# Performance work log

Hardware: AMD Instinct MI355X
Metric: run time of the kernel (lower is better)

## Reference

```python
import jax, jax.numpy as jnp
import numpy as np

# Module config (matches init_kwargs)
IC, OC, K, R, C, STRIDE = 128, 256, 3, 64, 64, 1
TAPS = 576
B = 16
BIAS_LEN = 128
H_OUT = (R - K) // STRIDE + 1  # 62
W_OUT = (C - K) // STRIDE + 1  # 62


def setup_inputs() -> dict:
    key = jax.random.key(0)
    k1, k2, k3 = jax.random.split(key, 3)
    rng = np.random.default_rng(0)
    # Per output channel, choose TAPS distinct (c, ky, kx) taps out of IC*K*K.
    all_taps = IC * K * K
    tap_ids = np.stack([rng.choice(all_taps, TAPS, replace=False) for _ in range(OC)])  # [OC, TAPS]
    c = tap_ids // (K * K)
    rem = tap_ids % (K * K)
    ky, kx = rem // K, rem % K
    # Flattened gather index into a [IC, R, C] image, exactly as the CUDA module builds it.
    image_weight_index = (c * (R * C) + ky * C + kx).astype(np.int32).reshape(-1)  # [OC*TAPS]
    filter_lengths = np.full(OC, TAPS, dtype=np.int32)
    start_points = (np.arange(OC, dtype=np.int64) * TAPS).astype(np.int32)
    bias_index = rng.choice(OC, BIAS_LEN, replace=False).astype(np.int32)
    return {
        "images": jax.random.normal(k1, (B, IC, R, C), jnp.float32),
        "weight_value": jax.random.normal(k2, (OC * TAPS,), jnp.float32) * 0.05,
        "image_weight_index": jnp.asarray(image_weight_index),
        "filter_lengths": jnp.asarray(filter_lengths),
        "start_points": jnp.asarray(start_points),
        "bias_index": jnp.asarray(bias_index),
        "bias_value": jax.random.normal(k3, (BIAS_LEN,), jnp.float32),
    }


def reference(images, weight_value, image_weight_index, filter_lengths, start_points, bias_index, bias_value):
    nnz = weight_value.shape[0]
    # Taps are stored contiguously per output channel (start_points = cumsum of filter_lengths).
    oc_ids = jnp.repeat(jnp.arange(OC), filter_lengths, total_repeat_length=nnz)
    # Decode flattened image index back to (in_channel, ky, kx).
    c = image_weight_index // (R * C)
    rem = image_weight_index % (R * C)
    ky, kx = rem // C, rem % C
    # Scatter sparse taps into a dense OIHW kernel; the gather-conv math is then
    # an exact VALID strided cross-correlation.
    W = jnp.zeros((OC, IC, K, K), images.dtype).at[oc_ids, c, ky, kx].add(weight_value)
    out = jax.lax.conv_general_dilated(
        images, W, window_strides=(STRIDE, STRIDE), padding="VALID",
        dimension_numbers=("NCHW", "OIHW", "NCHW"))  # [B, OC, H_OUT, W_OUT]
    # Conditional bias: channel oc gets bias_value[j] for each j with bias_index[j] == oc.
    bias = jnp.zeros((OC,), images.dtype).at[bias_index].add(bias_value)
    return out + bias[None, :, None, None]
```

## Files before the change

kernel.cpp:

```cpp
#include <hip/hip_runtime.h>
#include <stdint.h>

#define IC 128
#define OC 256
#define RR 64
#define CCOLS 64
#define HO 62
#define WO 62
#define NB 16

#define W9T_BYTES (9 * OC * IC * 2)
#define CHUNK_STRIDE 8192
#define LDS_TOTAL (49152 + 1024)

typedef __bf16 bf16x8 __attribute__((ext_vector_type(8)));
typedef float f32x16 __attribute__((ext_vector_type(16)));

__device__ __forceinline__ unsigned short f2bf(float f) {
    unsigned u = __builtin_bit_cast(unsigned, f);
    u += 0x7FFFu + ((u >> 16) & 1u);
    return (unsigned short)(u >> 16);
}

__global__ void prep_weights(const float* __restrict__ wv,
                             const int* __restrict__ iwi,
                             const int* __restrict__ flen,
                             const int* __restrict__ sp,
                             unsigned char* __restrict__ W9Tf,
                             const int* __restrict__ bias_index,
                             const float* __restrict__ bias_value,
                             float* __restrict__ bias_dense, int nbias) {
    if (blockIdx.x == OC) {
        int t = threadIdx.x;
        if (t < OC) bias_dense[t] = 0.f;
        __syncthreads();
        if (t < nbias) atomicAdd(&bias_dense[bias_index[t]], bias_value[t]);
        return;
    }
    const int oc = blockIdx.x;
    const int s = sp[oc];
    const int n = flen[oc];
    const int g = oc >> 5;
    for (int t = threadIdx.x; t < n; t += blockDim.x) {
        const int ix = iwi[s + t];
        const int c = ix >> 12;
        const int rem = ix & 4095;
        const int ky = rem >> 6, kx = rem & 63;
        const int kp = ky * 3 + kx;
        const int ck = c >> 4;
        const int khalf = (c >> 3) & 1;
        const int lane = (oc & 31) + (khalf << 5);
        const size_t off = (size_t)(kp * 8 + ck) * CHUNK_STRIDE +
                           g * 1024 + lane * 16 + (c & 7) * 2;
        *(unsigned short*)(W9Tf + off) = f2bf(wv[s + t]);
    }
}

#define KSTEP1(IDX, AV, VN, LGN)                                              \
  {                                                                           \
    if constexpr ((IDX) + 1 < 72) {                                           \
      constexpr int i1_ = (IDX) + 1;                                          \
      constexpr int kp1_ = i1_ >> 3, ck1_ = i1_ & 7;                          \
      constexpr int o1_ = (kp1_ / 3) * 16384 + ck1_ * 2048 + (kp1_ % 3) * 16; \
      asm volatile("ds_read_b128 %0, %1" : "=v"(b0n) : "v"(bB + o1_));        \
      asm volatile("ds_read_b128 %0, %1" : "=v"(b1n) : "v"(bB + o1_ + 512));  \
    }                                                                         \
    asm volatile("s_waitcnt vmcnt(" VN ") lgkmcnt(" LGN ")" : "+v"(AV));      \
    __builtin_amdgcn_sched_barrier(0);                                        \
    acc0 = __builtin_amdgcn_mfma_f32_32x32x16_bf16(AV, b0c, acc0, 0, 0, 0);   \
    acc1 = __builtin_amdgcn_mfma_f32_32x32x16_bf16(AV, b1c, acc1, 0, 0, 0);   \
    if constexpr ((IDX) + 4 < 72)                                             \
      asm volatile("global_load_dwordx4 %0, %1, off"                          \
                   : "=v"(AV)                                                 \
                   : "v"(pA + (size_t)((IDX) + 4) * CHUNK_STRIDE));           \
    if constexpr ((IDX) + 1 < 72) { b0c = b0n; b1c = b1n; }                   \
  }

#define K4(I) KSTEP1((I)+0, aS0, "3", "2") KSTEP1((I)+1, aS1, "3", "2") \
              KSTEP1((I)+2, aS2, "3", "2") KSTEP1((I)+3, aS3, "3", "2")

__global__ __launch_bounds__(512, 2) void conv_mfma(
    const float* __restrict__ images,
    const unsigned char* __restrict__ W9Tf,
    const float* __restrict__ bias_dense,
    float* __restrict__ out)
{
    const int y = blockIdx.x;
    const int b = blockIdx.y;
    const int t = threadIdx.x;
    const int w = t >> 6;
    const int l = t & 63;
    const int lm = l & 31;
    const int lhi = l >> 5;

    __shared__ unsigned char lds[LDS_TOTAL];

    const float* __restrict__ imgb = images + (size_t)b * (IC * RR * CCOLS);

    {
        const int xs = t & 63;
        const int oct = t >> 6;
        #pragma unroll
        for (int krow = 0; krow < 3; ++krow) {
            #pragma unroll
            for (int h = 0; h < 2; ++h) {
                const int o = oct + 8 * h;
                const int c0 = o * 8;
                const float* __restrict__ p =
                    imgb + (size_t)c0 * (RR * CCOLS) + (y + krow) * CCOLS + xs;
                unsigned v0, v1, v2, v3;
                v0 = (unsigned)f2bf(p[0])              | ((unsigned)f2bf(p[RR * CCOLS])     << 16);
                v1 = (unsigned)f2bf(p[2 * RR * CCOLS]) | ((unsigned)f2bf(p[3 * RR * CCOLS]) << 16);
                v2 = (unsigned)f2bf(p[4 * RR * CCOLS]) | ((unsigned)f2bf(p[5 * RR * CCOLS]) << 16);
                v3 = (unsigned)f2bf(p[6 * RR * CCOLS]) | ((unsigned)f2bf(p[7 * RR * CCOLS]) << 16);
                *(uint4*)(lds + krow * 16384 + o * 1024 + xs * 16) =
                    make_uint4(v0, v1, v2, v3);
            }
        }
    }

    const unsigned char* __restrict__ pA = W9Tf + w * 1024 + l * 16;
    const unsigned bB = (unsigned)(uintptr_t)(lds + lhi * 1024 + lm * 16);

    __syncthreads();

    bf16x8 aS0, aS1, aS2, aS3, b0c, b1c, b0n, b1n;
    asm volatile("global_load_dwordx4 %0, %1, off" : "=v"(aS0) : "v"(pA));
    asm volatile("global_load_dwordx4 %0, %1, off" : "=v"(aS1) : "v"(pA + CHUNK_STRIDE));
    asm volatile("global_load_dwordx4 %0, %1, off" : "=v"(aS2) : "v"(pA + 2 * CHUNK_STRIDE));
    asm volatile("global_load_dwordx4 %0, %1, off" : "=v"(aS3) : "v"(pA + 3 * CHUNK_STRIDE));
    asm volatile("ds_read_b128 %0, %1" : "=v"(b0c) : "v"(bB));
    asm volatile("ds_read_b128 %0, %1" : "=v"(b1c) : "v"(bB + 512u));

    f32x16 acc0 = {}, acc1 = {};

    K4(0) K4(4) K4(8) K4(12) K4(16) K4(20) K4(24) K4(28) K4(32)
    K4(36) K4(40) K4(44) K4(48) K4(52) K4(56) K4(60) K4(64)
    KSTEP1(68, aS0, "3", "2") KSTEP1(69, aS1, "2", "2")
    KSTEP1(70, aS2, "1", "2") KSTEP1(71, aS3, "0", "0")

    const int ocw = 32 * w;
    #pragma unroll
    for (int r = 0; r < 16; ++r) {
        const int oc = ocw + (r & 3) + 8 * (r >> 2) + 4 * lhi;
        const float bv = bias_dense[oc];
        const size_t ob = (((size_t)b * OC + oc) * HO + y) * WO;
        out[ob + lm] = acc0[r] + bv;
        if (lm < 30)
            out[ob + 32 + lm] = acc1[r] + bv;
    }
}

extern "C" void kernel_launch(void* const* d_in, const int* in_sizes, int n_in,
                              void* d_out, int out_size, void* d_ws, size_t ws_size,
                              hipStream_t stream) {
    const float* images             = (const float*)d_in[0];
    const float* weight_value       = (const float*)d_in[1];
    const int*   image_weight_index = (const int*)d_in[2];
    const int*   filter_lengths     = (const int*)d_in[3];
    const int*   start_points       = (const int*)d_in[4];
    const int*   bias_index         = (const int*)d_in[5];
    const float* bias_value         = (const float*)d_in[6];
    float* out = (float*)d_out;

    unsigned char* W9Tf = (unsigned char*)d_ws;
    float* bias_dense = (float*)((char*)d_ws + W9T_BYTES);

    hipMemsetAsync(d_ws, 0, W9T_BYTES, stream);
    prep_weights<<<OC + 1, 256, 0, stream>>>(weight_value, image_weight_index,
                                             filter_lengths, start_points, W9Tf,
                                             bias_index, bias_value, bias_dense,
                                             in_sizes[5]);

    dim3 grid(HO, NB);
    conv_mfma<<<grid, 512, 0, stream>>>(images, W9Tf, bias_dense, out);
}
```

Baseline: 64.74 us.

## Halve block size and give each wave two output-channel tiles

Blocks shrink from 512 to 256 threads, and each of the four waves now computes two 32-channel M tiles. Each LDS-read B fragment is reused across two MFMAs, which halves LDS traffic per MFMA and doubles the weight loads kept in flight per wave. LDS use per block drops slightly and launch bounds move to 3 blocks per CU. The cost is more accumulator and A registers per wave, and fewer waves per block to share the image-tile staging.

```diff
diff --git a/kernel.cpp b/kernel.cpp
--- a/kernel.cpp
+++ b/kernel.cpp
@@ -11,7 +11,7 @@
 
 #define W9T_BYTES (9 * OC * IC * 2)
 #define CHUNK_STRIDE 8192
-#define LDS_TOTAL (49152 + 1024)
+#define LDS_TOTAL 49216
 
 typedef __bf16 bf16x8 __attribute__((ext_vector_type(8)));
 typedef float f32x16 __attribute__((ext_vector_type(16)));
@@ -56,7 +56,7 @@
     }
 }
 
-#define KSTEP1(IDX, AV, VN, LGN)                                              \
+#define KSTEP1(IDX, AV0, AV1, VN, LGN)                                        \
   {                                                                           \
     if constexpr ((IDX) + 1 < 72) {                                           \
       constexpr int i1_ = (IDX) + 1;                                          \
@@ -65,21 +65,30 @@
       asm volatile("ds_read_b128 %0, %1" : "=v"(b0n) : "v"(bB + o1_));        \
       asm volatile("ds_read_b128 %0, %1" : "=v"(b1n) : "v"(bB + o1_ + 512));  \
     }                                                                         \
-    asm volatile("s_waitcnt vmcnt(" VN ") lgkmcnt(" LGN ")" : "+v"(AV));      \
+    asm volatile("s_waitcnt vmcnt(" VN ") lgkmcnt(" LGN ")"                   \
+                 : "+v"(AV0), "+v"(AV1));                                     \
     __builtin_amdgcn_sched_barrier(0);                                        \
-    acc0 = __builtin_amdgcn_mfma_f32_32x32x16_bf16(AV, b0c, acc0, 0, 0, 0);   \
-    acc1 = __builtin_amdgcn_mfma_f32_32x32x16_bf16(AV, b1c, acc1, 0, 0, 0);   \
-    if constexpr ((IDX) + 4 < 72)                                             \
+    c00 = __builtin_amdgcn_mfma_f32_32x32x16_bf16(AV0, b0c, c00, 0, 0, 0);    \
+    c10 = __builtin_amdgcn_mfma_f32_32x32x16_bf16(AV1, b0c, c10, 0, 0, 0);    \
+    c01 = __builtin_amdgcn_mfma_f32_32x32x16_bf16(AV0, b1c, c01, 0, 0, 0);    \
+    c11 = __builtin_amdgcn_mfma_f32_32x32x16_bf16(AV1, b1c, c11, 0, 0, 0);    \
+    if constexpr ((IDX) + 4 < 72) {                                           \
       asm volatile("global_load_dwordx4 %0, %1, off"                          \
-                   : "=v"(AV)                                                 \
-                   : "v"(pA + (size_t)((IDX) + 4) * CHUNK_STRIDE));           \
+                   : "=v"(AV0)                                                \
+                   : "v"(pA0 + (size_t)((IDX) + 4) * CHUNK_STRIDE));          \
+      asm volatile("global_load_dwordx4 %0, %1, off"                          \
+                   : "=v"(AV1)                                                \
+                   : "v"(pA1 + (size_t)((IDX) + 4) * CHUNK_STRIDE));          \
+    }                                                                         \
     if constexpr ((IDX) + 1 < 72) { b0c = b0n; b1c = b1n; }                   \
   }
 
-#define K4(I) KSTEP1((I)+0, aS0, "3", "2") KSTEP1((I)+1, aS1, "3", "2") \
-              KSTEP1((I)+2, aS2, "3", "2") KSTEP1((I)+3, aS3, "3", "2")
+#define K4(I) KSTEP1((I)+0, a0S0, a1S0, "6", "2") \
+              KSTEP1((I)+1, a0S1, a1S1, "6", "2") \
+              KSTEP1((I)+2, a0S2, a1S2, "6", "2") \
+              KSTEP1((I)+3, a0S3, a1S3, "6", "2")
 
-__global__ __launch_bounds__(512, 2) void conv_mfma(
+__global__ __launch_bounds__(256, 3) void conv_mfma(
     const float* __restrict__ images,
     const unsigned char* __restrict__ W9Tf,
     const float* __restrict__ bias_dense,
@@ -99,12 +108,12 @@
 
     {
         const int xs = t & 63;
-        const int oct = t >> 6;
+        const int og = t >> 6;
         #pragma unroll
         for (int krow = 0; krow < 3; ++krow) {
             #pragma unroll
-            for (int h = 0; h < 2; ++h) {
-                const int o = oct + 8 * h;
+            for (int h = 0; h < 4; ++h) {
+                const int o = og + 4 * h;
                 const int c0 = o * 8;
                 const float* __restrict__ p =
                     imgb + (size_t)c0 * (RR * CCOLS) + (y + krow) * CCOLS + xs;
@@ -119,35 +128,46 @@
         }
     }
 
-    const unsigned char* __restrict__ pA = W9Tf + w * 1024 + l * 16;
+    const unsigned char* __restrict__ pA0 = W9Tf + (2 * w + 0) * 1024 + l * 16;
+    const unsigned char* __restrict__ pA1 = W9Tf + (2 * w + 1) * 1024 + l * 16;
     const unsigned bB = (unsigned)(uintptr_t)(lds + lhi * 1024 + lm * 16);
 
     __syncthreads();
 
-    bf16x8 aS0, aS1, aS2, aS3, b0c, b1c, b0n, b1n;
-    asm volatile("global_load_dwordx4 %0, %1, off" : "=v"(aS0) : "v"(pA));
-    asm volatile("global_load_dwordx4 %0, %1, off" : "=v"(aS1) : "v"(pA + CHUNK_STRIDE));
-    asm volatile("global_load_dwordx4 %0, %1, off" : "=v"(aS2) : "v"(pA + 2 * CHUNK_STRIDE));
-    asm volatile("global_load_dwordx4 %0, %1, off" : "=v"(aS3) : "v"(pA + 3 * CHUNK_STRIDE));
+    bf16x8 a0S0, a0S1, a0S2, a0S3, a1S0, a1S1, a1S2, a1S3;
+    bf16x8 b0c, b1c, b0n, b1n;
+    asm volatile("global_load_dwordx4 %0, %1, off" : "=v"(a0S0) : "v"(pA0));
+    asm volatile("global_load_dwordx4 %0, %1, off" : "=v"(a1S0) : "v"(pA1));
+    asm volatile("global_load_dwordx4 %0, %1, off" : "=v"(a0S1) : "v"(pA0 + CHUNK_STRIDE));
+    asm volatile("global_load_dwordx4 %0, %1, off" : "=v"(a1S1) : "v"(pA1 + CHUNK_STRIDE));
+    asm volatile("global_load_dwordx4 %0, %1, off" : "=v"(a0S2) : "v"(pA0 + 2 * CHUNK_STRIDE));
+    asm volatile("global_load_dwordx4 %0, %1, off" : "=v"(a1S2) : "v"(pA1 + 2 * CHUNK_STRIDE));
+    asm volatile("global_load_dwordx4 %0, %1, off" : "=v"(a0S3) : "v"(pA0 + 3 * CHUNK_STRIDE));
+    asm volatile("global_load_dwordx4 %0, %1, off" : "=v"(a1S3) : "v"(pA1 + 3 * CHUNK_STRIDE));
     asm volatile("ds_read_b128 %0, %1" : "=v"(b0c) : "v"(bB));
     asm volatile("ds_read_b128 %0, %1" : "=v"(b1c) : "v"(bB + 512u));
 
-    f32x16 acc0 = {}, acc1 = {};
+    f32x16 c00 = {}, c01 = {}, c10 = {}, c11 = {};
 
     K4(0) K4(4) K4(8) K4(12) K4(16) K4(20) K4(24) K4(28) K4(32)
     K4(36) K4(40) K4(44) K4(48) K4(52) K4(56) K4(60) K4(64)
-    KSTEP1(68, aS0, "3", "2") KSTEP1(69, aS1, "2", "2")
-    KSTEP1(70, aS2, "1", "2") KSTEP1(71, aS3, "0", "0")
+    KSTEP1(68, a0S0, a1S0, "6", "2") KSTEP1(69, a0S1, a1S1, "4", "2")
+    KSTEP1(70, a0S2, a1S2, "2", "2") KSTEP1(71, a0S3, a1S3, "0", "0")
 
-    const int ocw = 32 * w;
     #pragma unroll
-    for (int r = 0; r < 16; ++r) {
-        const int oc = ocw + (r & 3) + 8 * (r >> 2) + 4 * lhi;
-        const float bv = bias_dense[oc];
-        const size_t ob = (((size_t)b * OC + oc) * HO + y) * WO;
-        out[ob + lm] = acc0[r] + bv;
-        if (lm < 30)
-            out[ob + 32 + lm] = acc1[r] + bv;
+    for (int m = 0; m < 2; ++m) {
+        const int ocw = (2 * w + m) * 32;
+        const f32x16 d0 = m ? c10 : c00;
+        const f32x16 d1 = m ? c11 : c01;
+        #pragma unroll
+        for (int r = 0; r < 16; ++r) {
+            const int oc = ocw + (r & 3) + 8 * (r >> 2) + 4 * lhi;
+            const float bv = bias_dense[oc];
+            const size_t ob = (((size_t)b * OC + oc) * HO + y) * WO;
+            out[ob + lm] = d0[r] + bv;
+            if (lm < 30)
+                out[ob + 32 + lm] = d1[r] + bv;
+        }
     }
 }
 
@@ -173,5 +193,5 @@
                                              in_sizes[5]);
 
     dim3 grid(HO, NB);
-    conv_mfma<<<grid, 512, 0, stream>>>(images, W9Tf, bias_dense, out);
+    conv_mfma<<<grid, 256, 0, stream>>>(images, W9Tf, bias_dense, out);
 }
```

New measurement: 65.38 us. No clear change (+1.0%).
